# Kernel tuning notes

Hardware: AMD Instinct MI355X
Metric: run time of the kernel (lower is better)

The kernel has to match this reference:

```python
import jax, jax.numpy as jnp
import numpy as np

D = 1024   # embd_dim
H = 4      # number of SelectiveAttentionModule heads (each full-dim)
B, S = 4, 2048


def _layernorm(x, g, b, eps=1e-5):
    mu = jnp.mean(x, axis=-1, keepdims=True)
    var = jnp.var(x, axis=-1, keepdims=True)
    return (x - mu) * jax.lax.rsqrt(var + eps) * g + b


def setup_inputs() -> dict:
    key = jax.random.key(0)
    ks = jax.random.split(key, 16)
    sd = 1.0 / np.sqrt(D)
    x = jax.random.normal(ks[0], (B, S, D), dtype=jnp.float32)
    # per-head Q/K/V projections, stacked over head dim H ([H, in, out] layout)
    Wq = jax.random.uniform(ks[1], (H, D, D), jnp.float32, -sd, sd)
    bq = jax.random.uniform(ks[2], (H, D), jnp.float32, -sd, sd)
    Wk = jax.random.uniform(ks[3], (H, D, D), jnp.float32, -sd, sd)
    bk = jax.random.uniform(ks[4], (H, D), jnp.float32, -sd, sd)
    Wv = jax.random.uniform(ks[5], (H, D, D), jnp.float32, -sd, sd)
    bv = jax.random.uniform(ks[6], (H, D), jnp.float32, -sd, sd)
    sd1 = 1.0 / np.sqrt(H * D)
    W1 = jax.random.uniform(ks[7], (H * D, D), jnp.float32, -sd1, sd1)  # [in, out]
    b1 = jax.random.uniform(ks[8], (D,), jnp.float32, -sd1, sd1)
    W2 = jax.random.uniform(ks[9], (D, D), jnp.float32, -sd, sd)
    b2 = jax.random.uniform(ks[10], (D,), jnp.float32, -sd, sd)
    g1 = jnp.ones((D,), jnp.float32)
    be1 = jnp.zeros((D,), jnp.float32)
    g2 = jnp.ones((D,), jnp.float32)
    be2 = jnp.zeros((D,), jnp.float32)
    return {"embedding_matrix": x, "Wq": Wq, "bq": bq, "Wk": Wk, "bk": bk,
            "Wv": Wv, "bv": bv, "W1": W1, "b1": b1, "g1": g1, "be1": be1,
            "W2": W2, "b2": b2, "g2": g2, "be2": be2}


def reference(embedding_matrix, Wq, bq, Wk, bk, Wv, bv, W1, b1, g1, be1, W2, b2, g2, be2):
    x = embedding_matrix  # [B, S, D]
    # batched per-head projections: [H, B, S, D]
    q = jnp.einsum('bsd,hde->hbse', x, Wq) + bq[:, None, None, :]
    k = jnp.einsum('bsd,hde->hbse', x, Wk) + bk[:, None, None, :]
    v = jnp.einsum('bsd,hde->hbse', x, Wv) + bv[:, None, None, :]
    scale = 1.0 / jnp.sqrt(jnp.asarray(D, x.dtype))
    scores = jnp.einsum('hbse,hbte->hbst', q, k) * scale  # [H, B, S, S]
    attn = jax.nn.softmax(scores, axis=-1)
    heads = jnp.einsum('hbst,hbte->hbse', attn, v)        # [H, B, S, D]
    # torch.cat([V1..V4], dim=-1) == heads reordered to [B, S, H*D]
    concat = jnp.moveaxis(heads, 0, 2).reshape(x.shape[0], x.shape[1], H * D)
    proj = concat @ W1 + b1                               # [B, S, D]
    y = _layernorm(x + proj, g1, be1)
    return _layernorm(y + (y @ W2 + b2), g2, be2)
```

## Files before the change

kernel.cpp:

```cpp
#include <hip/hip_runtime.h>

using u16 = unsigned short;
using u32 = unsigned int;
typedef __attribute__((ext_vector_type(8))) short s16x8;
typedef __attribute__((ext_vector_type(4))) float f32x4;

typedef uint4   __attribute__((may_alias)) uint4a;
typedef ushort4 __attribute__((may_alias)) ushort4a;
typedef float4  __attribute__((may_alias)) float4a;
typedef u16     __attribute__((may_alias)) u16a;
typedef s16x8   __attribute__((may_alias)) s16x8a;

#define D_ 1024
#define H_ 4
#define B_ 4
#define S_ 2048
#define M_ 8192

__device__ __forceinline__ float bf2f(u16 u) { return __uint_as_float(((u32)u) << 16); }
__device__ __forceinline__ u16 f2bf(float f) {
  u32 b = __float_as_uint(f);
  return (u16)((b + 0x7fffu + ((b >> 16) & 1u)) >> 16);
}

__device__ __forceinline__ void gload_lds16(const u16* g, u16* l) {
  __builtin_amdgcn_global_load_lds(
      (const __attribute__((address_space(1))) void*)g,
      (__attribute__((address_space(3))) void*)l, 16, 0, 0);
}

#define FENCE asm volatile("" ::: "memory")
#define BAR do { FENCE; __builtin_amdgcn_s_barrier(); FENCE; } while (0)
#define VMC4 asm volatile("s_waitcnt vmcnt(4)" ::: "memory")
#define VMC2 asm volatile("s_waitcnt vmcnt(2)" ::: "memory")

__device__ __forceinline__ void swz_decomp(int& x, int& y, int& z) {
  const int gx = gridDim.x, gy = gridDim.y;
  const int nwg = gx * gy * gridDim.z;
  const int flat = (blockIdx.z * gy + blockIdx.y) * gx + blockIdx.x;
  const int swz = (flat & 7) * (nwg >> 3) + (flat >> 3);
  const int t = swz >> 4, i = swz & 15;
  const int tiles_X = (gx * gridDim.z) >> 2;
  const int X = (t % tiles_X) * 4 + (i & 3);
  y = (t / tiles_X) * 4 + (i >> 2);
  z = X / gx;
  x = X % gx;
}

__global__ __launch_bounds__(256) void cvt_f32_bf16(const float* __restrict__ in,
                                                    u16* __restrict__ out, long n4) {
  long stride = (long)gridDim.x * blockDim.x;
  for (long i = (long)blockIdx.x * blockDim.x + threadIdx.x; i < n4; i += stride) {
    float4 v = ((const float4a*)in)[i];
    ushort4 o;
    o.x = f2bf(v.x); o.y = f2bf(v.y); o.z = f2bf(v.z); o.w = f2bf(v.w);
    ((ushort4a*)out)[i] = o;
  }
}

__global__ __launch_bounds__(256) void tcvt(const float* __restrict__ in,
                                            u16* __restrict__ out, int K, int N,
                                            long s_in, long s_out) {
  __shared__ float t[32][33];
  const int z = blockIdx.z;
  in += (long)z * s_in;
  out += (long)z * s_out;
  const int n0 = blockIdx.x * 32, k0 = blockIdx.y * 32;
  const int tx = threadIdx.x & 31, ty = threadIdx.x >> 5;
#pragma unroll
  for (int i = 0; i < 32; i += 8) t[ty + i][tx] = in[(long)(k0 + ty + i) * N + n0 + tx];
  __syncthreads();
#pragma unroll
  for (int i = 0; i < 32; i += 8)
    out[(long)(n0 + ty + i) * K + k0 + tx] = f2bf(t[tx][ty + i]);
}

__global__ __launch_bounds__(256) void biascat(const float* __restrict__ bq,
                                               const float* __restrict__ bk,
                                               const float* __restrict__ bv,
                                               float* __restrict__ o) {
  int i = blockIdx.x * 256 + threadIdx.x;
  float v = (i < 4096) ? bq[i] : ((i < 8192) ? bk[i - 4096] : bv[i - 8192]);
  o[i] = v;
}

__device__ __forceinline__ s16x8 lds_frag(const u16* buf, int r, int jc) {
  return *(const s16x8a*)&buf[(((r << 3) + (jc ^ (r & 7)))) << 3];
}
__device__ __forceinline__ void readA(const u16* Abuf, int q, int wr, int lane, s16x8 (&afr)[2][2]) {
#pragma unroll
  for (int il = 0; il < 2; ++il)
#pragma unroll
    for (int s = 0; s < 2; ++s)
      afr[il][s] = lds_frag(Abuf, wr * 128 + (q * 2 + il) * 16 + (lane & 15), 4 * s + (lane >> 4));
}

__device__ __forceinline__ void readB256(const u16* Bbuf, int wc, int lane, s16x8 (&bfr)[4][2]) {
#pragma unroll
  for (int j = 0; j < 4; ++j)
#pragma unroll
    for (int s = 0; s < 2; ++s)
      bfr[j][s] = lds_frag(Bbuf, wc * 64 + j * 16 + (lane & 15), 4 * s + (lane >> 4));
}
__device__ __forceinline__ void mfma_q256(const s16x8 (&afr)[2][2], const s16x8 (&bfr)[4][2],
                                          f32x4 (&acc)[8][4], int q) {
  __builtin_amdgcn_s_setprio(1);
#pragma unroll
  for (int s = 0; s < 2; ++s)
#pragma unroll
    for (int il = 0; il < 2; ++il)
#pragma unroll
      for (int j = 0; j < 4; ++j)
        acc[q * 2 + il][j] =
            __builtin_amdgcn_mfma_f32_16x16x32_bf16(afr[il][s], bfr[j][s], acc[q * 2 + il][j], 0, 0, 0);
  __builtin_amdgcn_s_setprio(0);
}

template <int MODE>
__device__ __forceinline__ void g256_body(
    const u16* __restrict__ A, const u16* __restrict__ Bm, u16* __restrict__ Cp,
    const float* __restrict__ bias, const float* __restrict__ bias2,
    float* __restrict__ dpart, int ldc, long sA, long sB, long sC) {
  __shared__ u16 Al[2][16384];
  __shared__ u16 Bl[2][16384];
  const int bx = blockIdx.x, by = blockIdx.y, z = blockIdx.z;
  A += (long)z * sA;
  Bm += (long)z * sB;
  const long coff = (long)z * sC;
  const int bm = by * 256, bn = bx * 256;
  const int tid = threadIdx.x;
  const int lane = tid & 63;
  const int w = tid >> 6;
  const int wr = w >> 2, wc = w & 3;
  f32x4 acc[8][4] = {};
  const int nt2 = D_ >> 7;

  auto stage = [&](const u16* src, int b0, u16* lbuf, int h, int kt) {
    const int k0 = kt << 6;
#pragma unroll
    for (int it = 0; it < 2; ++it) {
      int c = w * 128 + it * 64 + lane;
      int row = h * 128 + (c >> 3);
      int j = (c & 7) ^ (row & 7);
      gload_lds16(src + (long)(b0 + row) * D_ + (k0 + j * 8),
                  lbuf + ((h * 1024 + w * 128 + it * 64) << 3));
    }
  };

  stage(A, bm, Al[0], 0, 0);
  stage(A, bm, Al[0], 1, 0);
  stage(Bm, bn, Bl[0], 0, 0);
  stage(Bm, bn, Bl[0], 1, 0);
  stage(Bm, bn, Bl[1], 0, 1);
  stage(Bm, bn, Bl[1], 1, 1);
  VMC4;
  BAR;

  s16x8 bfr[4][2];
  for (int i2 = 0; i2 < nt2; ++i2) {
    const int t = i2 * 2;
    s16x8 afr[2][2];
    readB256(Bl[0], wc, lane, bfr);
    readA(Al[0], 0, wr, lane, afr);
    stage(A, bm, Al[1], 0, t + 1);
    BAR;
    mfma_q256(afr, bfr, acc, 0);
    BAR;
    readA(Al[0], 1, wr, lane, afr);
    stage(A, bm, Al[1], 1, t + 1);
    BAR;
    mfma_q256(afr, bfr, acc, 1);
    BAR;
    readA(Al[0], 2, wr, lane, afr);
    stage(Bm, bn, Bl[0], 0, t + 2);
    BAR;
    mfma_q256(afr, bfr, acc, 2);
    BAR;
    readA(Al[0], 3, wr, lane, afr);
    stage(Bm, bn, Bl[0], 1, t + 2);
    BAR;
    mfma_q256(afr, bfr, acc, 3);
    VMC4;
    BAR;
    readB256(Bl[1], wc, lane, bfr);
    readA(Al[1], 0, wr, lane, afr);
    stage(A, bm, Al[0], 0, t + 2);
    BAR;
    mfma_q256(afr, bfr, acc, 0);
    BAR;
    readA(Al[1], 1, wr, lane, afr);
    stage(A, bm, Al[0], 1, t + 2);
    BAR;
    mfma_q256(afr, bfr, acc, 1);
    BAR;
    readA(Al[1], 2, wr, lane, afr);
    stage(Bm, bn, Bl[1], 0, t + 3);
    BAR;
    mfma_q256(afr, bfr, acc, 2);
    BAR;
    readA(Al[1], 3, wr, lane, afr);
    stage(Bm, bn, Bl[1], 1, t + 3);
    BAR;
    mfma_q256(afr, bfr, acc, 3);
    VMC4;
    BAR;
  }

  if (MODE == 0) {
    const float* bb = (z == 1) ? bias2 : bias;
#pragma unroll
    for (int i = 0; i < 8; i++) {
      int mbase = bm + wr * 128 + i * 16 + ((lane >> 4) << 2);
#pragma unroll
      for (int j = 0; j < 4; j++) {
        int n = bn + wc * 64 + j * 16 + (lane & 15);
        float bv = bb[n];
#pragma unroll
        for (int r = 0; r < 4; r++)
          ((u16a*)Cp)[coff + (long)(mbase + r) * ldc + n] = f2bf(acc[i][j][r] + bv);
      }
    }
  } else {
#pragma unroll
    for (int i = 0; i < 8; i++) {
      int mbase = bm + wr * 128 + i * 16 + ((lane >> 4) << 2);
#pragma unroll
      for (int r = 0; r < 4; r++) {
        const int mm = mbase + r;
        float rowsum = 0.f;
#pragma unroll
        for (int j = 0; j < 4; j++) {
          int n = bn + wc * 64 + j * 16 + (lane & 15);
          float e = __expf(acc[i][j][r] * 0.03125f);
          ((u16a*)Cp)[coff + (long)mm * ldc + n] = f2bf(e);
          rowsum += e;
        }
        rowsum += __shfl_xor(rowsum, 1, 64);
        rowsum += __shfl_xor(rowsum, 2, 64);
        rowsum += __shfl_xor(rowsum, 4, 64);
        rowsum += __shfl_xor(rowsum, 8, 64);
        if ((lane & 15) == 0)
          dpart[((long)z * 32 + (bx * 4 + wc)) * S_ + mm] = rowsum;
      }
    }
  }
}

__global__ __launch_bounds__(512, 2) void kQK(
    const u16* __restrict__ A, const u16* __restrict__ Bm, u16* __restrict__ Cp,
    const float* __restrict__ bias, const float* __restrict__ bias2,
    float* __restrict__ dpart, int ldc, long sA, long sB, long sC) {
  g256_body<0>(A, Bm, Cp, bias, bias2, dpart, ldc, sA, sB, sC);
}
__global__ __launch_bounds__(512, 2) void kSC(
    const u16* __restrict__ A, const u16* __restrict__ Bm, u16* __restrict__ Cp,
    const float* __restrict__ bias, const float* __restrict__ bias2,
    float* __restrict__ dpart, int ldc, long sA, long sB, long sC) {
  g256_body<1>(A, Bm, Cp, bias, bias2, dpart, ldc, sA, sB, sC);
}

__device__ __forceinline__ void readB128(const u16* Bbuf, int wc, int lane, s16x8 (&bfr)[2][2]) {
#pragma unroll
  for (int j = 0; j < 2; ++j)
#pragma unroll
    for (int s = 0; s < 2; ++s)
      bfr[j][s] = lds_frag(Bbuf, wc * 32 + j * 16 + (lane & 15), 4 * s + (lane >> 4));
}
__device__ __forceinline__ void mfma_q128(const s16x8 (&afr)[2][2], const s16x8 (&bfr)[2][2],
                                          f32x4 (&acc)[8][2], int q) {
#pragma unroll
  for (int s = 0; s < 2; ++s)
#pragma unroll
    for (int il = 0; il < 2; ++il)
#pragma unroll
      for (int j = 0; j < 2; ++j)
        acc[q * 2 + il][j] =
            __builtin_amdgcn_mfma_f32_16x16x32_bf16(afr[il][s], bfr[j][s], acc[q * 2 + il][j], 0, 0, 0);
}

template <int OUT_MODE, int HAS_BIAS>
__device__ __forceinline__ void g256n_body(
    const u16* __restrict__ A, const u16* __restrict__ Bm, void* __restrict__ Cp,
    const float* __restrict__ bias, float* __restrict__ dpart,
    int K, int lda, int ldb, int ldc, long sA, long sB, long sC, float scale) {
  __shared__ u16 Al[2][16384];
  __shared__ u16 Bl[2][8192];
  __shared__ float sinv[256];
  int bx, by, z;
  swz_decomp(bx, by, z);
  A += (long)z * sA;
  Bm += (long)z * sB;
  const long coff = (long)z * sC;
  const int bm = by * 256, bn = bx * 128;
  const int tid = threadIdx.x;
  const int lane = tid & 63;
  const int w = tid >> 6;
  const int wr = w >> 2, wc = w & 3;
  f32x4 acc[8][2] = {};
  const int nt2 = K >> 7;

  auto stageA = [&](u16* Abuf, int h, int kt) {
    const int k0 = kt << 6;
#pragma unroll
    for (int it = 0; it < 2; ++it) {
      int c = w * 128 + it * 64 + lane;
      int row = h * 128 + (c >> 3);
      int j = (c & 7) ^ (row & 7);
      gload_lds16(A + (long)(bm + row) * lda + (k0 + j * 8),
                  Abuf + ((h * 1024 + w * 128 + it * 64) << 3));
    }
  };
  auto stageB = [&](u16* Bbuf, int kt) {
    const int k0 = kt << 6;
#pragma unroll
    for (int it = 0; it < 2; ++it) {
      int c = w * 128 + it * 64 + lane;
      int row = c >> 3;
      int j = (c & 7) ^ (row & 7);
      gload_lds16(Bm + (long)(bn + row) * ldb + (k0 + j * 8),
                  Bbuf + ((w * 128 + it * 64) << 3));
    }
  };

  stageA(Al[0], 0, 0);
  stageA(Al[0], 1, 0);
  stageB(Bl[0], 0);
  stageB(Bl[1], 1);
  VMC2;
  BAR;

  s16x8 bfr[2][2];
  for (int i2 = 0; i2 < nt2; ++i2) {
    const int t = i2 * 2;
    s16x8 afrA[2][2], afrB[2][2];
    readB128(Bl[0], wc, lane, bfr);
    readA(Al[0], 0, wr, lane, afrA);
    readA(Al[0], 1, wr, lane, afrB);
    stageA(Al[1], 0, t + 1);
    stageA(Al[1], 1, t + 1);
    BAR;
    __builtin_amdgcn_s_setprio(1);
    mfma_q128(afrA, bfr, acc, 0);
    mfma_q128(afrB, bfr, acc, 1);
    __builtin_amdgcn_s_setprio(0);
    BAR;
    readA(Al[0], 2, wr, lane, afrA);
    readA(Al[0], 3, wr, lane, afrB);
    stageB(Bl[0], t + 2);
    BAR;
    __builtin_amdgcn_s_setprio(1);
    mfma_q128(afrA, bfr, acc, 2);
    mfma_q128(afrB, bfr, acc, 3);
    __builtin_amdgcn_s_setprio(0);
    VMC2;
    BAR;
    readB128(Bl[1], wc, lane, bfr);
    readA(Al[1], 0, wr, lane, afrA);
    readA(Al[1], 1, wr, lane, afrB);
    stageA(Al[0], 0, t + 2);
    stageA(Al[0], 1, t + 2);
    BAR;
    __builtin_amdgcn_s_setprio(1);
    mfma_q128(afrA, bfr, acc, 0);
    mfma_q128(afrB, bfr, acc, 1);
    __builtin_amdgcn_s_setprio(0);
    BAR;
    readA(Al[1], 2, wr, lane, afrA);
    readA(Al[1], 3, wr, lane, afrB);
    stageB(Bl[1], t + 3);
    BAR;
    __builtin_amdgcn_s_setprio(1);
    mfma_q128(afrA, bfr, acc, 2);
    mfma_q128(afrB, bfr, acc, 3);
    __builtin_amdgcn_s_setprio(0);
    VMC2;
    BAR;
  }

  if (OUT_MODE == 5) {
    if (tid < 256) {
      const int row = bm + tid;
      float s = 0.f;
#pragma unroll
      for (int p = 0; p < 32; ++p) s += dpart[((long)z * 32 + p) * S_ + row];
      sinv[tid] = 1.0f / s;
    }
    __syncthreads();
#pragma unroll
    for (int i = 0; i < 8; i++) {
      int mloc = wr * 128 + i * 16 + ((lane >> 4) << 2);
      float inv[4];
#pragma unroll
      for (int r = 0; r < 4; r++) inv[r] = sinv[mloc + r];
#pragma unroll
      for (int j = 0; j < 2; j++) {
        int n = bn + wc * 32 + j * 16 + (lane & 15);
#pragma unroll
        for (int r = 0; r < 4; r++) {
          ((u16a*)Cp)[coff + (long)(bm + mloc + r) * ldc + n] = f2bf(acc[i][j][r] * inv[r]);
        }
      }
    }
    return;
  }
#pragma unroll
  for (int i = 0; i < 8; i++) {
    int mbase = bm + wr * 128 + i * 16 + ((lane >> 4) << 2);
#pragma unroll
    for (int j = 0; j < 2; j++) {
      int n = bn + wc * 32 + j * 16 + (lane & 15);
      float bv = 0.f;
      if (HAS_BIAS) bv = bias[n];
      if (OUT_MODE == 2) {
        ushort4 o;
        o.x = f2bf(acc[i][j][0] * scale + bv);
        o.y = f2bf(acc[i][j][1] * scale + bv);
        o.z = f2bf(acc[i][j][2] * scale + bv);
        o.w = f2bf(acc[i][j][3] * scale + bv);
        long idx = coff + (long)(mbase >> 11) * ((long)D_ * S_) + (long)n * S_ + (mbase & 2047);
        *(ushort4a*)&((u16a*)Cp)[idx] = o;
      } else {
#pragma unroll
        for (int r = 0; r < 4; r++) {
          float v = acc[i][j][r] * scale + bv;
          long idx = coff + (long)(mbase + r) * ldc + n;
          if (OUT_MODE == 1) {
            ((u16a*)Cp)[idx] = f2bf(v);
          } else if (OUT_MODE == 6) {
            u16a* Cb = (u16a*)Cp;
            Cb[idx] = f2bf(bf2f(Cb[idx]) + v);
          } else {
            ((float*)Cp)[idx] = v;
          }
        }
      }
    }
  }
}

#define G256N_ARGS \
    const u16* __restrict__ A, const u16* __restrict__ Bm, void* __restrict__ Cp, \
    const float* __restrict__ bias, float* __restrict__ dpart, \
    int K, int lda, int ldb, int ldc, long sA, long sB, long sC, float scale
#define G256N_FWD A, Bm, Cp, bias, dpart, K, lda, ldb, ldc, sA, sB, sC, scale

__global__ __launch_bounds__(512, 2) void kV(G256N_ARGS)   { g256n_body<2, 1>(G256N_FWD); }
__global__ __launch_bounds__(512, 2) void kPV(G256N_ARGS)  { g256n_body<5, 0>(G256N_FWD); }
__global__ __launch_bounds__(512, 2) void kW1a(G256N_ARGS) { g256n_body<1, 1>(G256N_FWD); }
__global__ __launch_bounds__(512, 2) void kW1b(G256N_ARGS) { g256n_body<6, 0>(G256N_FWD); }
__global__ __launch_bounds__(512, 2) void kW2(G256N_ARGS)  { g256n_body<0, 1>(G256N_FWD); }

template <int RBF>
__global__ __launch_bounds__(256) void ln_kernel(
    const float* __restrict__ X, const void* __restrict__ R,
    const float* __restrict__ g, const float* __restrict__ be,
    float* __restrict__ Y, u16* __restrict__ Yb) {
  const long row = blockIdx.x;
  const int t = threadIdx.x, lane = t & 63, w = t >> 6;
  const long base = row * 1024 + t * 4;
  float4 a = *(const float4a*)(X + base);
  float r0, r1, r2, r3;
  if (RBF) {
    ushort4 rb = *(const ushort4a*)((const u16*)R + base);
    r0 = bf2f(rb.x); r1 = bf2f(rb.y); r2 = bf2f(rb.z); r3 = bf2f(rb.w);
  } else {
    float4 b = *(const float4a*)((const float*)R + base);
    r0 = b.x; r1 = b.y; r2 = b.z; r3 = b.w;
  }
  float v0 = a.x + r0, v1 = a.y + r1, v2 = a.z + r2, v3 = a.w + r3;
  float s = v0 + v1 + v2 + v3;
  float q = v0 * v0 + v1 * v1 + v2 * v2 + v3 * v3;
#pragma unroll
  for (int o = 32; o > 0; o >>= 1) { s += __shfl_xor(s, o, 64); q += __shfl_xor(q, o, 64); }
  __shared__ float rs[4], rq[4];
  if (lane == 0) { rs[w] = s; rq[w] = q; }
  __syncthreads();
  s = rs[0] + rs[1] + rs[2] + rs[3];
  q = rq[0] + rq[1] + rq[2] + rq[3];
  const float mu = s * (1.f / 1024.f);
  const float var = q * (1.f / 1024.f) - mu * mu;
  const float rstd = rsqrtf(var + 1e-5f);
  float4 gv = *(const float4a*)(g + t * 4);
  float4 bv = *(const float4a*)(be + t * 4);
  float o0 = (v0 - mu) * rstd * gv.x + bv.x;
  float o1 = (v1 - mu) * rstd * gv.y + bv.y;
  float o2 = (v2 - mu) * rstd * gv.z + bv.z;
  float o3 = (v3 - mu) * rstd * gv.w + bv.w;
  float4 o4; o4.x = o0; o4.y = o1; o4.z = o2; o4.w = o3;
  *(float4a*)(Y + base) = o4;
  if (Yb) {
    ushort4 ob; ob.x = f2bf(o0); ob.y = f2bf(o1); ob.z = f2bf(o2); ob.w = f2bf(o3);
    *(ushort4a*)(Yb + base) = ob;
  }
}

extern "C" void kernel_launch(void* const* d_in, const int* in_sizes, int n_in,
                              void* d_out, int out_size, void* d_ws, size_t ws_size,
                              hipStream_t stream) {
  const float* x   = (const float*)d_in[0];
  const float* Wq  = (const float*)d_in[1];
  const float* bq  = (const float*)d_in[2];
  const float* Wk  = (const float*)d_in[3];
  const float* bk  = (const float*)d_in[4];
  const float* Wv  = (const float*)d_in[5];
  const float* bv  = (const float*)d_in[6];
  const float* W1  = (const float*)d_in[7];
  const float* b1  = (const float*)d_in[8];
  const float* g1  = (const float*)d_in[9];
  const float* be1 = (const float*)d_in[10];
  const float* W2  = (const float*)d_in[11];
  const float* b2  = (const float*)d_in[12];
  const float* g2  = (const float*)d_in[13];
  const float* be2 = (const float*)d_in[14];
  float* out = (float*)d_out;

  const size_t NEED = 170999808ULL;
  if (ws_size < NEED) return;
  char* ws = (char*)d_ws;
  u16* xb  = (u16*)(ws + 0L);
  u16* Wqt = (u16*)(ws + 16777216L);
  u16* Wkt = (u16*)(ws + 25165824L);
  u16* Wvt = (u16*)(ws + 33554432L);
  u16* W1t = (u16*)(ws + 41943040L);
  u16* W2t = (u16*)(ws + 50331648L);
  u16* Qh  = (u16*)(ws + 52428800L);
  u16* Kh  = (u16*)(ws + 69206016L);
  u16* Vt  = (u16*)(ws + 85983232L);
  u16* Sbh = (u16*)(ws + 102760448L);
  u16* Cc2 = (u16*)(ws + 136314880L);
  float* biasQKV = (float*)(ws + 169869312L);
  float* dpart   = (float*)(ws + 169951232L);
  u16* projb = (u16*)out;
  float* y  = (float*)Qh;
  u16*   yb = Vt;
  float* z2 = (float*)Cc2;

  dim3 blk(256), blk512(512);
  {
    long n4 = (long)M_ * D_ / 4;
    hipLaunchKernelGGL(cvt_f32_bf16, dim3(4096), blk, 0, stream, x, xb, n4);
  }
  hipLaunchKernelGGL(tcvt, dim3(32, 32, H_), blk, 0, stream, Wq, Wqt, D_, D_,
                     (long)D_ * D_, (long)D_ * D_);
  hipLaunchKernelGGL(tcvt, dim3(32, 32, H_), blk, 0, stream, Wk, Wkt, D_, D_,
                     (long)D_ * D_, (long)D_ * D_);
  hipLaunchKernelGGL(tcvt, dim3(32, 32, H_), blk, 0, stream, Wv, Wvt, D_, D_,
                     (long)D_ * D_, (long)D_ * D_);
  hipLaunchKernelGGL(tcvt, dim3(32, 128, 1), blk, 0, stream, W1, W1t, H_ * D_, D_, 0L, 0L);
  hipLaunchKernelGGL(tcvt, dim3(32, 32, 1), blk, 0, stream, W2, W2t, D_, D_, 0L, 0L);
  hipLaunchKernelGGL(biascat, dim3(48), blk, 0, stream, bq, bk, bv, biasQKV);

  for (int g = 0; g < 2; ++g) {
    for (int hh = 0; hh < 2; ++hh) {
      const int h = g * 2 + hh;
      const long wo = (long)h * D_ * D_;
      hipLaunchKernelGGL(kQK, dim3(4, 32, 2), blk512, 0, stream,
                         xb, Wqt + wo, Qh, biasQKV + (long)h * D_,
                         biasQKV + 4096 + (long)h * D_, (float*)nullptr,
                         D_, 0L, (long)H_ * D_ * D_, (long)M_ * D_);
      hipLaunchKernelGGL(kV, dim3(8, 32, 1), blk512, 0, stream,
                         xb, Wvt + wo, (void*)Vt, biasQKV + 8192 + (long)h * D_,
                         (float*)nullptr, D_, D_, D_, D_, 0L, 0L, 0L, 1.0f);
      hipLaunchKernelGGL(kSC, dim3(8, 8, B_), blk512, 0, stream,
                         Qh, Kh, Sbh, (const float*)nullptr, (const float*)nullptr,
                         dpart, S_, (long)S_ * D_, (long)S_ * D_, (long)S_ * S_);
      hipLaunchKernelGGL(kPV, dim3(8, 8, B_), blk512, 0, stream,
                         Sbh, Vt, (void*)(Cc2 + (long)hh * D_), (const float*)nullptr, dpart,
                         S_, S_, S_, 2 * D_,
                         (long)S_ * S_, (long)D_ * S_, (long)S_ * 2 * D_, 1.0f);
    }
    if (g == 0) {
      hipLaunchKernelGGL(kW1a, dim3(8, 32, 1), blk512, 0, stream,
                         Cc2, W1t + (long)g * 2 * D_, (void*)projb, b1, (float*)nullptr,
                         2 * D_, 2 * D_, H_ * D_, D_, 0L, 0L, 0L, 1.0f);
    } else {
      hipLaunchKernelGGL(kW1b, dim3(8, 32, 1), blk512, 0, stream,
                         Cc2, W1t + (long)g * 2 * D_, (void*)projb, (const float*)nullptr,
                         (float*)nullptr, 2 * D_, 2 * D_, H_ * D_, D_, 0L, 0L, 0L, 1.0f);
    }
  }

  hipLaunchKernelGGL((ln_kernel<1>), dim3(M_), blk, 0, stream, x, (const void*)projb,
                     g1, be1, y, yb);

  hipLaunchKernelGGL(kW2, dim3(8, 32, 1), blk512, 0, stream,
                     yb, W2t, (void*)z2, b2, (float*)nullptr,
                     D_, D_, D_, D_, 0L, 0L, 0L, 1.0f);

  hipLaunchKernelGGL((ln_kernel<0>), dim3(M_), blk, 0, stream, y, (const void*)z2,
                     g2, be2, out, (u16*)nullptr);
}
```

Before: 754.9 us.

## Use 256x256 tiles with split-K partials for PV, W1, W2 GEMMs

```diff
diff --git a/kernel.cpp b/kernel.cpp
--- a/kernel.cpp
+++ b/kernel.cpp
@@ -6,6 +6,7 @@
 typedef __attribute__((ext_vector_type(4))) float f32x4;
 
 typedef uint4   __attribute__((may_alias)) uint4a;
+typedef uint2   __attribute__((may_alias)) uint2a;
 typedef ushort4 __attribute__((may_alias)) ushort4a;
 typedef float4  __attribute__((may_alias)) float4a;
 typedef u16     __attribute__((may_alias)) u16a;
@@ -84,6 +85,37 @@
   o[i] = v;
 }
 
+__global__ __launch_bounds__(256) void pvfix(const u16* __restrict__ P,
+                                             const float* __restrict__ dpart,
+                                             u16* __restrict__ Cc2, int hh) {
+  const int r = blockIdx.x;
+  const int b = r >> 11, row = r & 2047;
+  const int tid = threadIdx.x;
+  __shared__ float sinv;
+  if (tid < 32) {
+    float v = dpart[((long)b * 32 + tid) * S_ + row];
+#pragma unroll
+    for (int o = 16; o > 0; o >>= 1) v += __shfl_xor(v, o, 64);
+    if (tid == 0) sinv = 1.0f / v;
+  }
+  __syncthreads();
+  const float inv = sinv;
+  const long base = (long)b * (S_ * (long)D_) + (long)row * D_ + tid * 4;
+  uint2 a0 = *(const uint2a*)(P + base);
+  uint2 a1 = *(const uint2a*)(P + 8388608L + base);
+  u16 o4[4];
+#pragma unroll
+  for (int j = 0; j < 4; ++j) {
+    u16 p0 = (u16)((j & 1) ? (((const u32*)&a0)[j >> 1] >> 16) : (((const u32*)&a0)[j >> 1] & 0xffff));
+    u16 p1 = (u16)((j & 1) ? (((const u32*)&a1)[j >> 1] >> 16) : (((const u32*)&a1)[j >> 1] & 0xffff));
+    o4[j] = f2bf((bf2f(p0) + bf2f(p1)) * inv);
+  }
+  uint2 ow;
+  ow.x = o4[0] | ((u32)o4[1] << 16);
+  ow.y = o4[2] | ((u32)o4[3] << 16);
+  *(uint2a*)(Cc2 + (long)r * (2 * D_) + hh * D_ + tid * 4) = ow;
+}
+
 __device__ __forceinline__ s16x8 lds_frag(const u16* buf, int r, int jc) {
   return *(const s16x8a*)&buf[(((r << 3) + (jc ^ (r & 7)))) << 3];
 }
@@ -120,39 +152,41 @@
 __device__ __forceinline__ void g256_body(
     const u16* __restrict__ A, const u16* __restrict__ Bm, u16* __restrict__ Cp,
     const float* __restrict__ bias, const float* __restrict__ bias2,
-    float* __restrict__ dpart, int ldc, long sA, long sB, long sC) {
+    float* __restrict__ dpart, int lda, int ldb, int ldc, int nK, int zdiv,
+    long sA1, long sA2, long sB1, long sB2, long sC1, long sC2) {
   __shared__ u16 Al[2][16384];
   __shared__ u16 Bl[2][16384];
   const int bx = blockIdx.x, by = blockIdx.y, z = blockIdx.z;
-  A += (long)z * sA;
-  Bm += (long)z * sB;
-  const long coff = (long)z * sC;
+  const int zq = z / zdiv, zr = z % zdiv;
+  A += zq * sA1 + zr * sA2;
+  Bm += zq * sB1 + zr * sB2;
+  const long coff = zq * sC1 + zr * sC2;
   const int bm = by * 256, bn = bx * 256;
   const int tid = threadIdx.x;
   const int lane = tid & 63;
   const int w = tid >> 6;
   const int wr = w >> 2, wc = w & 3;
   f32x4 acc[8][4] = {};
-  const int nt2 = D_ >> 7;
-
-  auto stage = [&](const u16* src, int b0, u16* lbuf, int h, int kt) {
+  const int nt2 = nK >> 7;
+
+  auto stage = [&](const u16* src, int ld, int b0, u16* lbuf, int h, int kt) {
     const int k0 = kt << 6;
 #pragma unroll
     for (int it = 0; it < 2; ++it) {
       int c = w * 128 + it * 64 + lane;
       int row = h * 128 + (c >> 3);
       int j = (c & 7) ^ (row & 7);
-      gload_lds16(src + (long)(b0 + row) * D_ + (k0 + j * 8),
+      gload_lds16(src + (long)(b0 + row) * ld + (k0 + j * 8),
                   lbuf + ((h * 1024 + w * 128 + it * 64) << 3));
     }
   };
 
-  stage(A, bm, Al[0], 0, 0);
-  stage(A, bm, Al[0], 1, 0);
-  stage(Bm, bn, Bl[0], 0, 0);
-  stage(Bm, bn, Bl[0], 1, 0);
-  stage(Bm, bn, Bl[1], 0, 1);
-  stage(Bm, bn, Bl[1], 1, 1);
+  stage(A, lda, bm, Al[0], 0, 0);
+  stage(A, lda, bm, Al[0], 1, 0);
+  stage(Bm, ldb, bn, Bl[0], 0, 0);
+  stage(Bm, ldb, bn, Bl[0], 1, 0);
+  stage(Bm, ldb, bn, Bl[1], 0, 1);
+  stage(Bm, ldb, bn, Bl[1], 1, 1);
   VMC4;
   BAR;
 
@@ -162,44 +196,44 @@
     s16x8 afr[2][2];
     readB256(Bl[0], wc, lane, bfr);
     readA(Al[0], 0, wr, lane, afr);
-    stage(A, bm, Al[1], 0, t + 1);
+    stage(A, lda, bm, Al[1], 0, t + 1);
     BAR;
     mfma_q256(afr, bfr, acc, 0);
     BAR;
     readA(Al[0], 1, wr, lane, afr);
-    stage(A, bm, Al[1], 1, t + 1);
+    stage(A, lda, bm, Al[1], 1, t + 1);
     BAR;
     mfma_q256(afr, bfr, acc, 1);
     BAR;
     readA(Al[0], 2, wr, lane, afr);
-    stage(Bm, bn, Bl[0], 0, t + 2);
+    stage(Bm, ldb, bn, Bl[0], 0, t + 2);
     BAR;
     mfma_q256(afr, bfr, acc, 2);
     BAR;
     readA(Al[0], 3, wr, lane, afr);
-    stage(Bm, bn, Bl[0], 1, t + 2);
+    stage(Bm, ldb, bn, Bl[0], 1, t + 2);
     BAR;
     mfma_q256(afr, bfr, acc, 3);
     VMC4;
     BAR;
     readB256(Bl[1], wc, lane, bfr);
     readA(Al[1], 0, wr, lane, afr);
-    stage(A, bm, Al[0], 0, t + 2);
+    stage(A, lda, bm, Al[0], 0, t + 2);
     BAR;
     mfma_q256(afr, bfr, acc, 0);
     BAR;
     readA(Al[1], 1, wr, lane, afr);
-    stage(A, bm, Al[0], 1, t + 2);
+    stage(A, lda, bm, Al[0], 1, t + 2);
     BAR;
     mfma_q256(afr, bfr, acc, 1);
     BAR;
     readA(Al[1], 2, wr, lane, afr);
-    stage(Bm, bn, Bl[1], 0, t + 3);
+    stage(Bm, ldb, bn, Bl[1], 0, t + 3);
     BAR;
     mfma_q256(afr, bfr, acc, 2);
     BAR;
     readA(Al[1], 3, wr, lane, afr);
-    stage(Bm, bn, Bl[1], 1, t + 3);
+    stage(Bm, ldb, bn, Bl[1], 1, t + 3);
     BAR;
     mfma_q256(afr, bfr, acc, 3);
     VMC4;
@@ -220,7 +254,7 @@
           ((u16a*)Cp)[coff + (long)(mbase + r) * ldc + n] = f2bf(acc[i][j][r] + bv);
       }
     }
-  } else {
+  } else if (MODE == 1) {
 #pragma unroll
     for (int i = 0; i < 8; i++) {
       int mbase = bm + wr * 128 + i * 16 + ((lane >> 4) << 2);
@@ -243,21 +277,43 @@
           dpart[((long)z * 32 + (bx * 4 + wc)) * S_ + mm] = rowsum;
       }
     }
-  }
-}
-
-__global__ __launch_bounds__(512, 2) void kQK(
-    const u16* __restrict__ A, const u16* __restrict__ Bm, u16* __restrict__ Cp,
-    const float* __restrict__ bias, const float* __restrict__ bias2,
-    float* __restrict__ dpart, int ldc, long sA, long sB, long sC) {
-  g256_body<0>(A, Bm, Cp, bias, bias2, dpart, ldc, sA, sB, sC);
-}
-__global__ __launch_bounds__(512, 2) void kSC(
-    const u16* __restrict__ A, const u16* __restrict__ Bm, u16* __restrict__ Cp,
-    const float* __restrict__ bias, const float* __restrict__ bias2,
-    float* __restrict__ dpart, int ldc, long sA, long sB, long sC) {
-  g256_body<1>(A, Bm, Cp, bias, bias2, dpart, ldc, sA, sB, sC);
-}
+  } else {
+#pragma unroll
+    for (int i = 0; i < 8; i++) {
+      int mbase = bm + wr * 128 + i * 16 + ((lane >> 4) << 2);
+#pragma unroll
+      for (int j = 0; j < 4; j++) {
+        int n = bn + wc * 64 + j * 16 + (lane & 15);
+        float bv = (MODE == 2 && bias && z == 0) ? bias[n] : 0.f;
+#pragma unroll
+        for (int r = 0; r < 4; r++) {
+          long idx = coff + (long)(mbase + r) * ldc + n;
+          if (MODE == 3) {
+            u16a* Cb = (u16a*)Cp;
+            Cb[idx] = f2bf(bf2f(Cb[idx]) + acc[i][j][r]);
+          } else {
+            ((u16a*)Cp)[idx] = f2bf(acc[i][j][r] + bv);
+          }
+        }
+      }
+    }
+  }
+}
+
+#define G256_ARGS \
+    const u16* __restrict__ A, const u16* __restrict__ Bm, u16* __restrict__ Cp, \
+    const float* __restrict__ bias, const float* __restrict__ bias2, \
+    float* __restrict__ dpart, int lda, int ldb, int ldc, int nK, int zdiv, \
+    long sA1, long sA2, long sB1, long sB2, long sC1, long sC2
+#define G256_FWD A, Bm, Cp, bias, bias2, dpart, lda, ldb, ldc, nK, zdiv, \
+    sA1, sA2, sB1, sB2, sC1, sC2
+
+__global__ __launch_bounds__(512, 2) void kQK(G256_ARGS)  { g256_body<0>(G256_FWD); }
+__global__ __launch_bounds__(512, 2) void kSC(G256_ARGS)  { g256_body<1>(G256_FWD); }
+__global__ __launch_bounds__(512, 2) void kPVs(G256_ARGS) { g256_body<2>(G256_FWD); }
+__global__ __launch_bounds__(512, 2) void kW1s(G256_ARGS) { g256_body<2>(G256_FWD); }
+__global__ __launch_bounds__(512, 2) void kW1r(G256_ARGS) { g256_body<3>(G256_FWD); }
+__global__ __launch_bounds__(512, 2) void kW2s(G256_ARGS) { g256_body<2>(G256_FWD); }
 
 __device__ __forceinline__ void readB128(const u16* Bbuf, int wc, int lane, s16x8 (&bfr)[2][2]) {
 #pragma unroll
@@ -278,26 +334,20 @@
             __builtin_amdgcn_mfma_f32_16x16x32_bf16(afr[il][s], bfr[j][s], acc[q * 2 + il][j], 0, 0, 0);
 }
 
-template <int OUT_MODE, int HAS_BIAS>
-__device__ __forceinline__ void g256n_body(
-    const u16* __restrict__ A, const u16* __restrict__ Bm, void* __restrict__ Cp,
-    const float* __restrict__ bias, float* __restrict__ dpart,
-    int K, int lda, int ldb, int ldc, long sA, long sB, long sC, float scale) {
+__global__ __launch_bounds__(512, 2) void kV(
+    const u16* __restrict__ A, const u16* __restrict__ Bm, u16* __restrict__ Cp,
+    const float* __restrict__ bias) {
   __shared__ u16 Al[2][16384];
   __shared__ u16 Bl[2][8192];
-  __shared__ float sinv[256];
   int bx, by, z;
   swz_decomp(bx, by, z);
-  A += (long)z * sA;
-  Bm += (long)z * sB;
-  const long coff = (long)z * sC;
   const int bm = by * 256, bn = bx * 128;
   const int tid = threadIdx.x;
   const int lane = tid & 63;
   const int w = tid >> 6;
   const int wr = w >> 2, wc = w & 3;
   f32x4 acc[8][2] = {};
-  const int nt2 = K >> 7;
+  const int nt2 = D_ >> 7;
 
   auto stageA = [&](u16* Abuf, int h, int kt) {
     const int k0 = kt << 6;
@@ -306,7 +356,7 @@
       int c = w * 128 + it * 64 + lane;
       int row = h * 128 + (c >> 3);
       int j = (c & 7) ^ (row & 7);
-      gload_lds16(A + (long)(bm + row) * lda + (k0 + j * 8),
+      gload_lds16(A + (long)(bm + row) * D_ + (k0 + j * 8),
                   Abuf + ((h * 1024 + w * 128 + it * 64) << 3));
     }
   };
@@ -317,7 +367,7 @@
       int c = w * 128 + it * 64 + lane;
       int row = c >> 3;
       int j = (c & 7) ^ (row & 7);
-      gload_lds16(Bm + (long)(bn + row) * ldb + (k0 + j * 8),
+      gload_lds16(Bm + (long)(bn + row) * D_ + (k0 + j * 8),
                   Bbuf + ((w * 128 + it * 64) << 3));
     }
   };
@@ -377,97 +427,38 @@
     BAR;
   }
 
-  if (OUT_MODE == 5) {
-    if (tid < 256) {
-      const int row = bm + tid;
-      float s = 0.f;
-#pragma unroll
-      for (int p = 0; p < 32; ++p) s += dpart[((long)z * 32 + p) * S_ + row];
-      sinv[tid] = 1.0f / s;
-    }
-    __syncthreads();
-#pragma unroll
-    for (int i = 0; i < 8; i++) {
-      int mloc = wr * 128 + i * 16 + ((lane >> 4) << 2);
-      float inv[4];
-#pragma unroll
-      for (int r = 0; r < 4; r++) inv[r] = sinv[mloc + r];
-#pragma unroll
-      for (int j = 0; j < 2; j++) {
-        int n = bn + wc * 32 + j * 16 + (lane & 15);
-#pragma unroll
-        for (int r = 0; r < 4; r++) {
-          ((u16a*)Cp)[coff + (long)(bm + mloc + r) * ldc + n] = f2bf(acc[i][j][r] * inv[r]);
-        }
-      }
-    }
-    return;
-  }
 #pragma unroll
   for (int i = 0; i < 8; i++) {
     int mbase = bm + wr * 128 + i * 16 + ((lane >> 4) << 2);
 #pragma unroll
     for (int j = 0; j < 2; j++) {
       int n = bn + wc * 32 + j * 16 + (lane & 15);
-      float bv = 0.f;
-      if (HAS_BIAS) bv = bias[n];
-      if (OUT_MODE == 2) {
-        ushort4 o;
-        o.x = f2bf(acc[i][j][0] * scale + bv);
-        o.y = f2bf(acc[i][j][1] * scale + bv);
-        o.z = f2bf(acc[i][j][2] * scale + bv);
-        o.w = f2bf(acc[i][j][3] * scale + bv);
-        long idx = coff + (long)(mbase >> 11) * ((long)D_ * S_) + (long)n * S_ + (mbase & 2047);
-        *(ushort4a*)&((u16a*)Cp)[idx] = o;
-      } else {
-#pragma unroll
-        for (int r = 0; r < 4; r++) {
-          float v = acc[i][j][r] * scale + bv;
-          long idx = coff + (long)(mbase + r) * ldc + n;
-          if (OUT_MODE == 1) {
-            ((u16a*)Cp)[idx] = f2bf(v);
-          } else if (OUT_MODE == 6) {
-            u16a* Cb = (u16a*)Cp;
-            Cb[idx] = f2bf(bf2f(Cb[idx]) + v);
-          } else {
-            ((float*)Cp)[idx] = v;
-          }
-        }
-      }
-    }
-  }
-}
-
-#define G256N_ARGS \
-    const u16* __restrict__ A, const u16* __restrict__ Bm, void* __restrict__ Cp, \
-    const float* __restrict__ bias, float* __restrict__ dpart, \
-    int K, int lda, int ldb, int ldc, long sA, long sB, long sC, float scale
-#define G256N_FWD A, Bm, Cp, bias, dpart, K, lda, ldb, ldc, sA, sB, sC, scale
-
-__global__ __launch_bounds__(512, 2) void kV(G256N_ARGS)   { g256n_body<2, 1>(G256N_FWD); }
-__global__ __launch_bounds__(512, 2) void kPV(G256N_ARGS)  { g256n_body<5, 0>(G256N_FWD); }
-__global__ __launch_bounds__(512, 2) void kW1a(G256N_ARGS) { g256n_body<1, 1>(G256N_FWD); }
-__global__ __launch_bounds__(512, 2) void kW1b(G256N_ARGS) { g256n_body<6, 0>(G256N_FWD); }
-__global__ __launch_bounds__(512, 2) void kW2(G256N_ARGS)  { g256n_body<0, 1>(G256N_FWD); }
-
-template <int RBF>
-__global__ __launch_bounds__(256) void ln_kernel(
-    const float* __restrict__ X, const void* __restrict__ R,
+      float bv = bias[n];
+      ushort4 o;
+      o.x = f2bf(acc[i][j][0] + bv);
+      o.y = f2bf(acc[i][j][1] + bv);
+      o.z = f2bf(acc[i][j][2] + bv);
+      o.w = f2bf(acc[i][j][3] + bv);
+      long idx = (long)(mbase >> 11) * ((long)D_ * S_) + (long)n * S_ + (mbase & 2047);
+      *(ushort4a*)&((u16a*)Cp)[idx] = o;
+    }
+  }
+}
+
+__global__ __launch_bounds__(256) void ln2r(
+    const float* __restrict__ X, const u16* __restrict__ R0, const u16* __restrict__ R1,
     const float* __restrict__ g, const float* __restrict__ be,
     float* __restrict__ Y, u16* __restrict__ Yb) {
   const long row = blockIdx.x;
   const int t = threadIdx.x, lane = t & 63, w = t >> 6;
   const long base = row * 1024 + t * 4;
   float4 a = *(const float4a*)(X + base);
-  float r0, r1, r2, r3;
-  if (RBF) {
-    ushort4 rb = *(const ushort4a*)((const u16*)R + base);
-    r0 = bf2f(rb.x); r1 = bf2f(rb.y); r2 = bf2f(rb.z); r3 = bf2f(rb.w);
-  } else {
-    float4 b = *(const float4a*)((const float*)R + base);
-    r0 = b.x; r1 = b.y; r2 = b.z; r3 = b.w;
-  }
-  float v0 = a.x + r0, v1 = a.y + r1, v2 = a.z + r2, v3 = a.w + r3;
+  ushort4 r0 = *(const ushort4a*)(R0 + base);
+  ushort4 r1 = *(const ushort4a*)(R1 + base);
+  float v0 = a.x + bf2f(r0.x) + bf2f(r1.x);
+  float v1 = a.y + bf2f(r0.y) + bf2f(r1.y);
+  float v2 = a.z + bf2f(r0.z) + bf2f(r1.z);
+  float v3 = a.w + bf2f(r0.w) + bf2f(r1.w);
   float s = v0 + v1 + v2 + v3;
   float q = v0 * v0 + v1 * v1 + v2 * v2 + v3 * v3;
 #pragma unroll
@@ -530,10 +521,13 @@
   u16* Cc2 = (u16*)(ws + 136314880L);
   float* biasQKV = (float*)(ws + 169869312L);
   float* dpart   = (float*)(ws + 169951232L);
-  u16* projb = (u16*)out;
+  u16* Ppart = Qh;
+  u16* pa = (u16*)out;
+  u16* pb = (u16*)out + 8388608L;
+  u16* z2a = Cc2;
+  u16* z2b = Cc2 + 8388608L;
   float* y  = (float*)Qh;
   u16*   yb = Vt;
-  float* z2 = (float*)Cc2;
 
   dim3 blk(256), blk512(512);
   {
@@ -557,36 +551,40 @@
       hipLaunchKernelGGL(kQK, dim3(4, 32, 2), blk512, 0, stream,
                          xb, Wqt + wo, Qh, biasQKV + (long)h * D_,
                          biasQKV + 4096 + (long)h * D_, (float*)nullptr,
-                         D_, 0L, (long)H_ * D_ * D_, (long)M_ * D_);
+                         D_, D_, D_, D_, 1,
+                         0L, 0L, (long)H_ * D_ * D_, 0L, (long)M_ * D_, 0L);
       hipLaunchKernelGGL(kV, dim3(8, 32, 1), blk512, 0, stream,
-                         xb, Wvt + wo, (void*)Vt, biasQKV + 8192 + (long)h * D_,
-                         (float*)nullptr, D_, D_, D_, D_, 0L, 0L, 0L, 1.0f);
+                         xb, Wvt + wo, Vt, biasQKV + 8192 + (long)h * D_);
       hipLaunchKernelGGL(kSC, dim3(8, 8, B_), blk512, 0, stream,
                          Qh, Kh, Sbh, (const float*)nullptr, (const float*)nullptr,
-                         dpart, S_, (long)S_ * D_, (long)S_ * D_, (long)S_ * S_);
-      hipLaunchKernelGGL(kPV, dim3(8, 8, B_), blk512, 0, stream,
-                         Sbh, Vt, (void*)(Cc2 + (long)hh * D_), (const float*)nullptr, dpart,
-                         S_, S_, S_, 2 * D_,
-                         (long)S_ * S_, (long)D_ * S_, (long)S_ * 2 * D_, 1.0f);
+                         dpart, D_, D_, S_, D_, 1,
+                         (long)S_ * D_, 0L, (long)S_ * D_, 0L, (long)S_ * S_, 0L);
+      hipLaunchKernelGGL(kPVs, dim3(4, 8, 8), blk512, 0, stream,
+                         Sbh, Vt, Ppart, (const float*)nullptr, (const float*)nullptr,
+                         (float*)nullptr, S_, S_, D_, D_, 2,
+                         (long)S_ * S_, 1024L, (long)D_ * S_, 1024L,
+                         (long)S_ * D_, (long)B_ * S_ * D_);
+      hipLaunchKernelGGL(pvfix, dim3(M_), blk, 0, stream, Ppart, dpart, Cc2, hh);
     }
     if (g == 0) {
-      hipLaunchKernelGGL(kW1a, dim3(8, 32, 1), blk512, 0, stream,
-                         Cc2, W1t + (long)g * 2 * D_, (void*)projb, b1, (float*)nullptr,
-                         2 * D_, 2 * D_, H_ * D_, D_, 0L, 0L, 0L, 1.0f);
+      hipLaunchKernelGGL(kW1s, dim3(4, 32, 2), blk512, 0, stream,
+                         Cc2, W1t + (long)g * 2 * D_, pa, b1, (const float*)nullptr,
+                         (float*)nullptr, 2 * D_, H_ * D_, D_, D_, 1,
+                         1024L, 0L, 1024L, 0L, 8388608L, 0L);
     } else {
-      hipLaunchKernelGGL(kW1b, dim3(8, 32, 1), blk512, 0, stream,
-                         Cc2, W1t + (long)g * 2 * D_, (void*)projb, (const float*)nullptr,
-                         (float*)nullptr, 2 * D_, 2 * D_, H_ * D_, D_, 0L, 0L, 0L, 1.0f);
-    }
-  }
-
-  hipLaunchKernelGGL((ln_kernel<1>), dim3(M_), blk, 0, stream, x, (const void*)projb,
-                     g1, be1, y, yb);
-
-  hipLaunchKernelGGL(kW2, dim3(8, 32, 1), blk512, 0, stream,
-                     yb, W2t, (void*)z2, b2, (float*)nullptr,
-                     D_, D_, D_, D_, 0L, 0L, 0L, 1.0f);
-
-  hipLaunchKernelGGL((ln_kernel<0>), dim3(M_), blk, 0, stream, y, (const void*)z2,
-                     g2, be2, out, (u16*)nullptr);
-}
+      hipLaunchKernelGGL(kW1r, dim3(4, 32, 2), blk512, 0, stream,
+                         Cc2, W1t + (long)g * 2 * D_, pa, (const float*)nullptr,
+                         (const float*)nullptr, (float*)nullptr, 2 * D_, H_ * D_, D_, D_, 1,
+                         1024L, 0L, 1024L, 0L, 8388608L, 0L);
+    }
+  }
+
+  hipLaunchKernelGGL(ln2r, dim3(M_), blk, 0, stream, x, pa, pb, g1, be1, y, yb);
+
+  hipLaunchKernelGGL(kW2s, dim3(4, 32, 2), blk512, 0, stream,
+                     yb, W2t, z2a, b2, (const float*)nullptr, (float*)nullptr,
+                     D_, D_, D_, 512, 1,
+                     512L, 0L, 512L, 0L, 8388608L, 0L);
+
+  hipLaunchKernelGGL(ln2r, dim3(M_), blk, 0, stream, y, z2a, z2b, g2, be2, out, (u16*)nullptr);
+}
```

Result: slower. 827.7 us (+9.6%).
